# Performance work log

Measured on AMD Instinct MI355X. Metric: run time of the kernel, lower is better.

The kernel has to match this reference:

```python
import jax, jax.numpy as jnp
import numpy as np

N_NODES = 50000
N_EDGES = 600000
IN_DIM = 128
OUT_DIM = 128
NEG_SLOPE = 0.2
LN_EPS = 1e-5


def setup_inputs() -> dict:
    key = jax.random.key(0)
    ks = jax.random.split(key, 8)
    x = jax.random.normal(ks[0], (N_NODES, IN_DIM), dtype=jnp.float32)
    edge_index = jax.random.randint(ks[1], (2, N_EDGES), 0, N_NODES, dtype=jnp.int64)
    glorot = float(np.sqrt(6.0 / (IN_DIM + OUT_DIM)))
    W_l = jax.random.uniform(ks[2], (IN_DIM, OUT_DIM), jnp.float32, -glorot, glorot)
    W_r = jax.random.uniform(ks[3], (IN_DIM, OUT_DIM), jnp.float32, -glorot, glorot)
    att = jax.random.uniform(ks[4], (OUT_DIM,), jnp.float32, -glorot, glorot)
    bias = jnp.zeros((OUT_DIM,), jnp.float32)
    ln_gamma = jnp.ones((OUT_DIM,), jnp.float32)
    ln_beta = jnp.zeros((OUT_DIM,), jnp.float32)
    return {"x": x, "edge_index": edge_index, "W_l": W_l, "W_r": W_r,
            "att": att, "bias": bias, "ln_gamma": ln_gamma, "ln_beta": ln_beta}


def _gatv2_ln(x, edge_index, W_l, W_r, att, bias, ln_gamma, ln_beta):
    N = x.shape[0]
    # add self loops (PyG GATv2Conv default add_self_loops=True)
    loop = jnp.arange(N, dtype=edge_index.dtype)
    src = jnp.concatenate([edge_index[0], loop])  # [E+N]
    dst = jnp.concatenate([edge_index[1], loop])
    x_l = x @ W_l  # [N, D] transformed source features
    x_r = x @ W_r  # [N, D] transformed target features
    # GATv2 edge score: e_ij = a^T LeakyReLU(x_l[src] + x_r[dst])
    h = jax.nn.leaky_relu(x_l[src] + x_r[dst], NEG_SLOPE)  # [E+N, D]
    e = h @ att  # [E+N]
    # segment softmax over incoming edges of each dst node
    m = jax.lax.stop_gradient(jax.ops.segment_max(e, dst, num_segments=N))
    ex = jnp.exp(e - m[dst])
    denom = jax.ops.segment_sum(ex, dst, num_segments=N)
    alpha = ex / denom[dst]  # [E+N] (denom > 0 thanks to self loops)
    # weighted scatter-add aggregation (dropout=0.1 is inference no-op)
    out = jax.ops.segment_sum(alpha[:, None] * x_l[src], dst, num_segments=N)
    out = out + bias  # heads=1, concat=False -> mean over 1 head = identity
    # LayerNorm over feature dim
    mu = jnp.mean(out, axis=-1, keepdims=True)
    var = jnp.var(out, axis=-1, keepdims=True)
    return (out - mu) * jax.lax.rsqrt(var + LN_EPS) * ln_gamma + ln_beta


def reference(x, edge_index, W_l, W_r, att, bias, ln_gamma, ln_beta):
    return _gatv2_ln(x, edge_index, W_l, W_r, att, bias, ln_gamma, ln_beta)
```

## Files before the change

kernel.cpp:

```cpp
#include <hip/hip_runtime.h>
#include <hip/hip_bf16.h>


constexpr int NN  = 50000;
constexpr int NE  = 600000;
constexpr int D   = 128;
constexpr int CAP = 64;
constexpr int MT  = 80;
constexpr int GEMM_THREADS = 320;

typedef __attribute__((ext_vector_type(8))) short bf16x8;
typedef __attribute__((ext_vector_type(4))) float f32x4;

__device__ __forceinline__ ushort f2bf(float f) {
  uint u = __builtin_bit_cast(uint, f);
  return (ushort)((u + 0x7FFFu + ((u >> 16) & 1u)) >> 16);
}
__device__ __forceinline__ float bflo(uint u) { return __builtin_bit_cast(float, u << 16); }
__device__ __forceinline__ float bfhi(uint u) { return __builtin_bit_cast(float, u & 0xFFFF0000u); }
__device__ __forceinline__ void unpack8(uint4 u, float* v) {
  v[0] = bflo(u.x); v[1] = bfhi(u.x);
  v[2] = bflo(u.y); v[3] = bfhi(u.y);
  v[4] = bflo(u.z); v[5] = bfhi(u.z);
  v[6] = bflo(u.w); v[7] = bfhi(u.w);
}

__global__ __launch_bounds__(256) void k_wpack(const float* __restrict__ Wl,
    const float* __restrict__ Wr, ushort* __restrict__ wpk) {
  const int t = blockIdx.x * 256 + threadIdx.x;
  if (t >= 2 * 4 * 8 * 64) return;
  const int lane = t & 63;
  const int ct   = (t >> 6) & 7;
  const int ks   = (t >> 9) & 3;
  const int wh   = t >> 11;
  const float* W = wh ? Wr : Wl;
  const int c  = ct * 16 + (lane & 15);
  const int k0 = ks * 32 + (lane >> 4) * 8;
  ushort v[8];
#pragma unroll
  for (int j = 0; j < 8; ++j) v[j] = f2bf(W[(k0 + j) * D + c]);
  *(bf16x8*)&wpk[(size_t)t * 8] = *(bf16x8*)v;
}

__global__ __launch_bounds__(GEMM_THREADS) void k_gemm(const float* __restrict__ x,
    const ushort* __restrict__ wpk, ushort* __restrict__ xl,
    ushort* __restrict__ xr) {
  __shared__ __align__(16) ushort axs[MT * D];
  const int t = threadIdx.x;
  const int row0 = blockIdx.x * MT;
  for (int ch = t; ch < MT * 16; ch += GEMM_THREADS) {
    const int r = ch >> 4, kc = ch & 15;
    const float4* src = (const float4*)&x[(size_t)(row0 + r) * D + kc * 8];
    const float4 f0 = src[0], f1 = src[1];
    ushort pk[8];
    pk[0] = f2bf(f0.x); pk[1] = f2bf(f0.y); pk[2] = f2bf(f0.z); pk[3] = f2bf(f0.w);
    pk[4] = f2bf(f1.x); pk[5] = f2bf(f1.y); pk[6] = f2bf(f1.z); pk[7] = f2bf(f1.w);
    uint byte = (uint)(r * 256 + kc * 16);
    byte ^= (uint)((r & 7) << 4);
    *(bf16x8*)((char*)axs + byte) = *(bf16x8*)pk;
  }
  __syncthreads();
  const int w = t >> 6, l = t & 63;
  f32x4 accl[8], accr[8];
#pragma unroll
  for (int ct = 0; ct < 8; ++ct) { accl[ct] = (f32x4)0.f; accr[ct] = (f32x4)0.f; }
  const bf16x8* wv = (const bf16x8*)wpk;
  const int rloc = w * 16 + (l & 15);
#pragma unroll
  for (int ks = 0; ks < 4; ++ks) {
    uint byte = (uint)(rloc * 256 + ks * 64 + ((l >> 4) << 4));
    byte ^= (uint)((rloc & 7) << 4);
    const bf16x8 a = *(const bf16x8*)((const char*)axs + byte);
#pragma unroll
    for (int ct = 0; ct < 8; ++ct) {
      const bf16x8 bl = wv[((0 * 4 + ks) * 8 + ct) * 64 + l];
      const bf16x8 br = wv[((1 * 4 + ks) * 8 + ct) * 64 + l];
      accl[ct] = __builtin_amdgcn_mfma_f32_16x16x32_bf16(a, bl, accl[ct], 0, 0, 0);
      accr[ct] = __builtin_amdgcn_mfma_f32_16x16x32_bf16(a, br, accr[ct], 0, 0, 0);
    }
  }
  const int rl0 = w * 16 + ((l >> 4) << 2);
  const int cl  = l & 15;
#pragma unroll
  for (int ct = 0; ct < 8; ++ct) {
    const int col = ct * 16 + cl;
#pragma unroll
    for (int i = 0; i < 4; ++i) {
      const size_t o = (size_t)(row0 + rl0 + i) * D + col;
      xl[o] = f2bf(accl[ct][i]);
      xr[o] = f2bf(accr[ct][i]);
    }
  }
}

__global__ __launch_bounds__(256) void k_fill(const int* __restrict__ ei,
    int* __restrict__ cnt, int* __restrict__ eidx) {
  const int e = blockIdx.x * 256 + threadIdx.x;
  if (e < NE) {
    const int src = ei[e];
    const int dst = ei[NE + e];
    const int pos = atomicAdd(&cnt[dst], 1);
    if (pos < CAP) eidx[dst * CAP + pos] = src;
  }
}

__global__ __launch_bounds__(256) void k_node(const int* __restrict__ cnt,
    const int* __restrict__ eidx,
    const ushort* __restrict__ xl, const ushort* __restrict__ xr,
    const float* __restrict__ att, const float* __restrict__ bias,
    const float* __restrict__ gamma, const float* __restrict__ beta,
    float* __restrict__ out) {
  const int n = blockIdx.x * 4 + (threadIdx.x >> 6);
  const int lane = threadIdx.x & 63;
  const int eg = lane & 3;
  const int ls = lane >> 2;
  const int d0 = ls * 8;
  constexpr float LOG2E = 1.4426950408889634f;

  float vr[8], av[8], vs[8];
  unpack8(*(const uint4*)&xr[(uint)n * D + d0], vr);
  unpack8(*(const uint4*)&xl[(uint)n * D + d0], vs);
  *(float4*)&av[0] = *(const float4*)&att[d0];
  *(float4*)&av[4] = *(const float4*)&att[d0 + 4];

  const int m    = min(cnt[n], CAP);
  const int base = n * CAP;

  float ss = 0.f;
#pragma unroll
  for (int j = 0; j < 8; ++j) {
    float h = vs[j] + vr[j];
    h = fmaxf(h, 0.2f * h);
    ss = fmaf(h, av[j], ss);
  }
  ss += __shfl_xor(ss, 4);
  ss += __shfl_xor(ss, 8);
  ss += __shfl_xor(ss, 16);
  ss += __shfl_xor(ss, 32);
  const float eself = exp2f(ss * LOG2E);

  float acc[8] = {0.f,0.f,0.f,0.f,0.f,0.f,0.f,0.f};
  float den = 0.f;

  int s1 = (eg < m) ? eidx[base + eg] : n;
  uint4 u = *(const uint4*)&xl[(uint)s1 * D + d0];
  s1 = (4 + eg < m) ? eidx[base + 4 + eg] : n;

  for (int p0 = 0; p0 < m; p0 += 4) {
    uint4 un = *(const uint4*)&xl[(uint)s1 * D + d0];
    const int pe2 = p0 + 8 + eg;
    const int s2 = (pe2 < m) ? eidx[base + pe2] : n;
    const bool act = (p0 + eg < m);
    float v[8];
    unpack8(u, v);
    float h0, h1;
    h0 = v[0] + vr[0]; h0 = fmaxf(h0, 0.2f * h0);
    h1 = v[1] + vr[1]; h1 = fmaxf(h1, 0.2f * h1);
    float t0 = fmaf(h0, av[0], h1 * av[1]);
    h0 = v[2] + vr[2]; h0 = fmaxf(h0, 0.2f * h0);
    h1 = v[3] + vr[3]; h1 = fmaxf(h1, 0.2f * h1);
    float t1 = fmaf(h0, av[2], h1 * av[3]);
    h0 = v[4] + vr[4]; h0 = fmaxf(h0, 0.2f * h0);
    h1 = v[5] + vr[5]; h1 = fmaxf(h1, 0.2f * h1);
    float t2 = fmaf(h0, av[4], h1 * av[5]);
    h0 = v[6] + vr[6]; h0 = fmaxf(h0, 0.2f * h0);
    h1 = v[7] + vr[7]; h1 = fmaxf(h1, 0.2f * h1);
    float t3 = fmaf(h0, av[6], h1 * av[7]);
    float s = (t0 + t1) + (t2 + t3);
    s += __shfl_xor(s, 4);
    s += __shfl_xor(s, 8);
    s += __shfl_xor(s, 16);
    s += __shfl_xor(s, 32);
    const float e = act ? exp2f(s * LOG2E) : 0.f;
    den += e;
#pragma unroll
    for (int j = 0; j < 8; ++j) acc[j] = fmaf(e, v[j], acc[j]);
    u = un; s1 = s2;
  }
#pragma unroll
  for (int j = 0; j < 8; ++j) {
    acc[j] += __shfl_xor(acc[j], 1);
    acc[j] += __shfl_xor(acc[j], 2);
  }
  den += __shfl_xor(den, 1);
  den += __shfl_xor(den, 2);
  den += eself;
#pragma unroll
  for (int j = 0; j < 8; ++j) acc[j] = fmaf(eself, vs[j], acc[j]);
  const float inv = 1.0f / den;

  float o[8];
  {
    const float4 b0 = *(const float4*)&bias[d0];
    const float4 b1 = *(const float4*)&bias[d0 + 4];
    o[0] = fmaf(acc[0], inv, b0.x); o[1] = fmaf(acc[1], inv, b0.y);
    o[2] = fmaf(acc[2], inv, b0.z); o[3] = fmaf(acc[3], inv, b0.w);
    o[4] = fmaf(acc[4], inv, b1.x); o[5] = fmaf(acc[5], inv, b1.y);
    o[6] = fmaf(acc[6], inv, b1.z); o[7] = fmaf(acc[7], inv, b1.w);
  }
  float sm = 0.f, sq = 0.f;
#pragma unroll
  for (int j = 0; j < 8; ++j) { sm += o[j]; sq = fmaf(o[j], o[j], sq); }
  sm += __shfl_xor(sm, 4);  sq += __shfl_xor(sq, 4);
  sm += __shfl_xor(sm, 8);  sq += __shfl_xor(sq, 8);
  sm += __shfl_xor(sm, 16); sq += __shfl_xor(sq, 16);
  sm += __shfl_xor(sm, 32); sq += __shfl_xor(sq, 32);
  const float mean = sm * (1.0f / D);
  const float var  = sq * (1.0f / D) - mean * mean;
  const float rstd = rsqrtf(var + 1e-5f);
  if (eg == 0) {
    const float4 g0 = *(const float4*)&gamma[d0];
    const float4 g1 = *(const float4*)&gamma[d0 + 4];
    const float4 be0 = *(const float4*)&beta[d0];
    const float4 be1 = *(const float4*)&beta[d0 + 4];
    float4 o0, o1;
    o0.x = (o[0] - mean) * rstd * g0.x + be0.x;
    o0.y = (o[1] - mean) * rstd * g0.y + be0.y;
    o0.z = (o[2] - mean) * rstd * g0.z + be0.z;
    o0.w = (o[3] - mean) * rstd * g0.w + be0.w;
    o1.x = (o[4] - mean) * rstd * g1.x + be1.x;
    o1.y = (o[5] - mean) * rstd * g1.y + be1.y;
    o1.z = (o[6] - mean) * rstd * g1.z + be1.z;
    o1.w = (o[7] - mean) * rstd * g1.w + be1.w;
    *(float4*)&out[(size_t)n * D + d0]     = o0;
    *(float4*)&out[(size_t)n * D + d0 + 4] = o1;
  }
}

extern "C" void kernel_launch(void* const* d_in, const int* in_sizes, int n_in,
                              void* d_out, int out_size, void* d_ws, size_t ws_size,
                              hipStream_t stream) {
  const float* x     = (const float*)d_in[0];
  const int*   ei    = (const int*)d_in[1];
  const float* Wl    = (const float*)d_in[2];
  const float* Wr    = (const float*)d_in[3];
  const float* att   = (const float*)d_in[4];
  const float* bias  = (const float*)d_in[5];
  const float* gamma = (const float*)d_in[6];
  const float* beta  = (const float*)d_in[7];
  float* out = (float*)d_out;

  char* ws = (char*)d_ws;
  ushort* xl   = (ushort*)ws;
  ushort* xr   = xl + (size_t)NN * D;
  int*    eidx = (int*)(xr + (size_t)NN * D);
  int*    cnt  = eidx + (size_t)NN * CAP;
  ushort* wpk  = (ushort*)(cnt + NN);

  hipMemsetAsync(cnt, 0, NN * sizeof(int), stream);
  k_wpack<<<16, 256, 0, stream>>>(Wl, Wr, wpk);
  k_gemm<<<NN / MT, GEMM_THREADS, 0, stream>>>(x, wpk, xl, xr);
  k_fill<<<(NE + 255) / 256, 256, 0, stream>>>(ei, cnt, eidx);
  k_node<<<NN / 4, 256, 0, stream>>>(cnt, eidx, xl, xr, att, bias, gamma,
                                     beta, out);
}
```

Before: 181.7 us.

## Fuse setup kernels, co-schedule GEMM with edge fill, unroll gather by two

```diff
diff --git a/kernel.cpp b/kernel.cpp
--- a/kernel.cpp
+++ b/kernel.cpp
@@ -8,6 +8,8 @@
 constexpr int CAP = 64;
 constexpr int MT  = 80;
 constexpr int GEMM_THREADS = 320;
+constexpr int GEMM_BLOCKS  = NN / MT;
+constexpr int FILL_BLOCKS  = (NE / 4 + GEMM_THREADS - 1) / GEMM_THREADS;
 
 typedef __attribute__((ext_vector_type(8))) short bf16x8;
 typedef __attribute__((ext_vector_type(4))) float f32x4;
@@ -25,10 +27,15 @@
   v[6] = bflo(u.w); v[7] = bfhi(u.w);
 }
 
-__global__ __launch_bounds__(256) void k_wpack(const float* __restrict__ Wl,
-    const float* __restrict__ Wr, ushort* __restrict__ wpk) {
+__global__ __launch_bounds__(256) void k_setup(const float* __restrict__ Wl,
+    const float* __restrict__ Wr, ushort* __restrict__ wpk,
+    int* __restrict__ cnt) {
+  if (blockIdx.x >= 16) {
+    const int i = (blockIdx.x - 16) * 256 + threadIdx.x;
+    if (i < NN) cnt[i] = 0;
+    return;
+  }
   const int t = blockIdx.x * 256 + threadIdx.x;
-  if (t >= 2 * 4 * 8 * 64) return;
   const int lane = t & 63;
   const int ct   = (t >> 6) & 7;
   const int ks   = (t >> 9) & 3;
@@ -42,9 +49,23 @@
   *(bf16x8*)&wpk[(size_t)t * 8] = *(bf16x8*)v;
 }
 
-__global__ __launch_bounds__(GEMM_THREADS) void k_gemm(const float* __restrict__ x,
+__global__ __launch_bounds__(GEMM_THREADS) void k_mega(const float* __restrict__ x,
     const ushort* __restrict__ wpk, ushort* __restrict__ xl,
-    ushort* __restrict__ xr) {
+    ushort* __restrict__ xr, const int* __restrict__ ei,
+    int* __restrict__ cnt, int* __restrict__ eidx) {
+  if (blockIdx.x >= GEMM_BLOCKS) {
+    const int e0 = ((blockIdx.x - GEMM_BLOCKS) * GEMM_THREADS + threadIdx.x) * 4;
+    if (e0 < NE) {
+      const int4 s4 = *(const int4*)&ei[e0];
+      const int4 d4 = *(const int4*)&ei[NE + e0];
+      int pos;
+      pos = atomicAdd(&cnt[d4.x], 1); if (pos < CAP) eidx[d4.x * CAP + pos] = s4.x;
+      pos = atomicAdd(&cnt[d4.y], 1); if (pos < CAP) eidx[d4.y * CAP + pos] = s4.y;
+      pos = atomicAdd(&cnt[d4.z], 1); if (pos < CAP) eidx[d4.z * CAP + pos] = s4.z;
+      pos = atomicAdd(&cnt[d4.w], 1); if (pos < CAP) eidx[d4.w * CAP + pos] = s4.w;
+    }
+    return;
+  }
   __shared__ __align__(16) ushort axs[MT * D];
   const int t = threadIdx.x;
   const int row0 = blockIdx.x * MT;
@@ -93,17 +114,6 @@
   }
 }
 
-__global__ __launch_bounds__(256) void k_fill(const int* __restrict__ ei,
-    int* __restrict__ cnt, int* __restrict__ eidx) {
-  const int e = blockIdx.x * 256 + threadIdx.x;
-  if (e < NE) {
-    const int src = ei[e];
-    const int dst = ei[NE + e];
-    const int pos = atomicAdd(&cnt[dst], 1);
-    if (pos < CAP) eidx[dst * CAP + pos] = src;
-  }
-}
-
 __global__ __launch_bounds__(256) void k_node(const int* __restrict__ cnt,
     const int* __restrict__ eidx,
     const ushort* __restrict__ xl, const ushort* __restrict__ xr,
@@ -142,40 +152,60 @@
   float acc[8] = {0.f,0.f,0.f,0.f,0.f,0.f,0.f,0.f};
   float den = 0.f;
 
-  int s1 = (eg < m) ? eidx[base + eg] : n;
-  uint4 u = *(const uint4*)&xl[(uint)s1 * D + d0];
-  s1 = (4 + eg < m) ? eidx[base + 4 + eg] : n;
-
-  for (int p0 = 0; p0 < m; p0 += 4) {
-    uint4 un = *(const uint4*)&xl[(uint)s1 * D + d0];
-    const int pe2 = p0 + 8 + eg;
-    const int s2 = (pe2 < m) ? eidx[base + pe2] : n;
-    const bool act = (p0 + eg < m);
-    float v[8];
-    unpack8(u, v);
-    float h0, h1;
-    h0 = v[0] + vr[0]; h0 = fmaxf(h0, 0.2f * h0);
-    h1 = v[1] + vr[1]; h1 = fmaxf(h1, 0.2f * h1);
-    float t0 = fmaf(h0, av[0], h1 * av[1]);
-    h0 = v[2] + vr[2]; h0 = fmaxf(h0, 0.2f * h0);
-    h1 = v[3] + vr[3]; h1 = fmaxf(h1, 0.2f * h1);
-    float t1 = fmaf(h0, av[2], h1 * av[3]);
-    h0 = v[4] + vr[4]; h0 = fmaxf(h0, 0.2f * h0);
-    h1 = v[5] + vr[5]; h1 = fmaxf(h1, 0.2f * h1);
-    float t2 = fmaf(h0, av[4], h1 * av[5]);
-    h0 = v[6] + vr[6]; h0 = fmaxf(h0, 0.2f * h0);
-    h1 = v[7] + vr[7]; h1 = fmaxf(h1, 0.2f * h1);
-    float t3 = fmaf(h0, av[6], h1 * av[7]);
-    float s = (t0 + t1) + (t2 + t3);
-    s += __shfl_xor(s, 4);
-    s += __shfl_xor(s, 8);
-    s += __shfl_xor(s, 16);
-    s += __shfl_xor(s, 32);
-    const float e = act ? exp2f(s * LOG2E) : 0.f;
-    den += e;
-#pragma unroll
-    for (int j = 0; j < 8; ++j) acc[j] = fmaf(e, v[j], acc[j]);
-    u = un; s1 = s2;
+  int sA = (eg < m)     ? eidx[base + eg]     : n;
+  int sB = (4 + eg < m) ? eidx[base + 4 + eg] : n;
+  uint4 uA = *(const uint4*)&xl[(uint)sA * D + d0];
+  uint4 uB = *(const uint4*)&xl[(uint)sB * D + d0];
+
+  for (int p0 = 0; p0 < m; p0 += 8) {
+    const int pA = p0 + 8 + eg, pB = p0 + 12 + eg;
+    const int nA = (pA < m) ? eidx[base + pA] : n;
+    const int nB = (pB < m) ? eidx[base + pB] : n;
+    const uint4 vA = *(const uint4*)&xl[(uint)nA * D + d0];
+    const uint4 vB = *(const uint4*)&xl[(uint)nB * D + d0];
+
+    const bool actA = (p0 + eg < m);
+    const bool actB = (p0 + 4 + eg < m);
+    float a[8], b[8];
+    unpack8(uA, a);
+    unpack8(uB, b);
+    float h0, h1, g0, g1;
+    h0 = a[0] + vr[0]; h0 = fmaxf(h0, 0.2f * h0);
+    h1 = a[1] + vr[1]; h1 = fmaxf(h1, 0.2f * h1);
+    g0 = b[0] + vr[0]; g0 = fmaxf(g0, 0.2f * g0);
+    g1 = b[1] + vr[1]; g1 = fmaxf(g1, 0.2f * g1);
+    float tA0 = fmaf(h0, av[0], h1 * av[1]);
+    float tB0 = fmaf(g0, av[0], g1 * av[1]);
+    h0 = a[2] + vr[2]; h0 = fmaxf(h0, 0.2f * h0);
+    h1 = a[3] + vr[3]; h1 = fmaxf(h1, 0.2f * h1);
+    g0 = b[2] + vr[2]; g0 = fmaxf(g0, 0.2f * g0);
+    g1 = b[3] + vr[3]; g1 = fmaxf(g1, 0.2f * g1);
+    float tA1 = fmaf(h0, av[2], h1 * av[3]);
+    float tB1 = fmaf(g0, av[2], g1 * av[3]);
+    h0 = a[4] + vr[4]; h0 = fmaxf(h0, 0.2f * h0);
+    h1 = a[5] + vr[5]; h1 = fmaxf(h1, 0.2f * h1);
+    g0 = b[4] + vr[4]; g0 = fmaxf(g0, 0.2f * g0);
+    g1 = b[5] + vr[5]; g1 = fmaxf(g1, 0.2f * g1);
+    float tA2 = fmaf(h0, av[4], h1 * av[5]);
+    float tB2 = fmaf(g0, av[4], g1 * av[5]);
+    h0 = a[6] + vr[6]; h0 = fmaxf(h0, 0.2f * h0);
+    h1 = a[7] + vr[7]; h1 = fmaxf(h1, 0.2f * h1);
+    g0 = b[6] + vr[6]; g0 = fmaxf(g0, 0.2f * g0);
+    g1 = b[7] + vr[7]; g1 = fmaxf(g1, 0.2f * g1);
+    float tA3 = fmaf(h0, av[6], h1 * av[7]);
+    float tB3 = fmaf(g0, av[6], g1 * av[7]);
+    float sA_ = (tA0 + tA1) + (tA2 + tA3);
+    float sB_ = (tB0 + tB1) + (tB2 + tB3);
+    sA_ += __shfl_xor(sA_, 4);  sB_ += __shfl_xor(sB_, 4);
+    sA_ += __shfl_xor(sA_, 8);  sB_ += __shfl_xor(sB_, 8);
+    sA_ += __shfl_xor(sA_, 16); sB_ += __shfl_xor(sB_, 16);
+    sA_ += __shfl_xor(sA_, 32); sB_ += __shfl_xor(sB_, 32);
+    const float eA = actA ? exp2f(sA_ * LOG2E) : 0.f;
+    const float eB = actB ? exp2f(sB_ * LOG2E) : 0.f;
+    den += eA + eB;
+#pragma unroll
+    for (int j = 0; j < 8; ++j) acc[j] = fmaf(eA, a[j], fmaf(eB, b[j], acc[j]));
+    uA = vA; uB = vB;
   }
 #pragma unroll
   for (int j = 0; j < 8; ++j) {
@@ -247,10 +277,9 @@
   int*    cnt  = eidx + (size_t)NN * CAP;
   ushort* wpk  = (ushort*)(cnt + NN);
 
-  hipMemsetAsync(cnt, 0, NN * sizeof(int), stream);
-  k_wpack<<<16, 256, 0, stream>>>(Wl, Wr, wpk);
-  k_gemm<<<NN / MT, GEMM_THREADS, 0, stream>>>(x, wpk, xl, xr);
-  k_fill<<<(NE + 255) / 256, 256, 0, stream>>>(ei, cnt, eidx);
+  k_setup<<<16 + (NN + 255) / 256, 256, 0, stream>>>(Wl, Wr, wpk, cnt);
+  k_mega<<<GEMM_BLOCKS + FILL_BLOCKS, GEMM_THREADS, 0, stream>>>(
+      x, wpk, xl, xr, ei, cnt, eidx);
   k_node<<<NN / 4, 256, 0, stream>>>(cnt, eidx, xl, xr, att, bias, gamma,
                                      beta, out);
 }
```

After: 176.0 us. 3.1% less time.
